# Kernel optimization log

Measured on AMD Instinct MI355X. Metric: run time of the kernel, lower is better.

The kernel has to match this reference:

```python
import jax, jax.numpy as jnp
import numpy as np
from jax import lax

B, S, D_MODEL, H, P = 16, 2048, 512, 8, 128
DEPTH = D_MODEL // H          # 64
C = (S + P - 1) // P          # chunk_size = 16


def _build_table():
    # table[R-1, c, :] = indices of positions assigned to cluster c when R real tokens,
    # padded with R (the padded zero-row index when R == S, else first pad position).
    table = np.zeros((S, P, C), dtype=np.int32)
    cols = np.arange(C)
    for R in range(1, S + 1):
        assign = np.minimum(np.arange(R) * P // R, P - 1)  # nondecreasing
        starts = np.searchsorted(assign, np.arange(P), side='left')
        ends = np.searchsorted(assign, np.arange(P), side='right')
        cand = starts[:, None] + cols[None, :]
        table[R - 1] = np.where(cand < ends[:, None], cand, R)
    return table


def setup_inputs() -> dict:
    key = jax.random.key(0)
    ks = jax.random.split(key, 12)
    def glorot(k, shp):
        fan = shp[-2] + shp[-1]
        return jax.random.normal(k, shp, jnp.float32) * np.sqrt(2.0 / fan).astype(np.float32)
    x = jax.random.normal(ks[0], (B, S, D_MODEL), jnp.float32)
    lengths = jax.random.randint(ks[1], (B,), S // 2, S + 1)
    mask = jnp.arange(S)[None, :] < lengths[:, None]
    return dict(
        x=x, mask=mask,
        wq=glorot(ks[2], (D_MODEL, D_MODEL)),
        wk=glorot(ks[3], (D_MODEL, D_MODEL)),
        wv=glorot(ks[4], (D_MODEL, D_MODEL)),
        e_w=glorot(ks[5], (H, P, C)),
        f_w=glorot(ks[6], (H, P, C)),
        ck1=glorot(ks[7], (1, P, 1, 1)), cb1=jnp.zeros((1,), jnp.float32),
        ck3=glorot(ks[8], (3, P, 1, 1)), cb3=jnp.zeros((1,), jnp.float32),
        ck5=glorot(ks[9], (5, P, 1, 1)), cb5=jnp.zeros((1,), jnp.float32),
        dw=glorot(ks[10], (D_MODEL, D_MODEL)),
        db=jnp.zeros((D_MODEL,), jnp.float32),
        table=jnp.asarray(_build_table()),
    )


def _conv_same(z, kern, bias):
    # z: (N, S, P, 1), kern: (h, P, 1, 1); Keras Conv2D padding='same', stride 1
    return lax.conv_general_dilated(
        z, kern, window_strides=(1, 1), padding='SAME',
        dimension_numbers=('NHWC', 'HWIO', 'NHWC')) + bias


def _forward(x, mask, wq, wk, wv, e_w, f_w, ck1, cb1, ck3, cb3, ck5, cb5, dw, db, table):
    b = x.shape[0]
    split = lambda t: t.reshape(b, S, H, DEPTH).transpose(0, 2, 1, 3)  # (B,H,S,depth)
    q = split(x @ wq)
    k = split(x @ wk)
    v = split(x @ wv)
    pad = ((0, 0), (0, 0), (0, 1), (0, 0))
    k = jnp.pad(k, pad)  # (B,H,S+1,depth) zero pad row at index S
    v = jnp.pad(v, pad)
    real_counts = jnp.clip(jnp.sum(mask.astype(jnp.int32), axis=1), 1, S)
    pos = table[real_counts - 1]                  # (B,P,C) per-batch cluster index table
    gather = jax.vmap(lambda t, idx: t[:, idx])   # gather over seq axis per batch
    k_ch = gather(k, pos)                          # (B,H,P,C,depth)
    v_ch = gather(v, pos)
    k_proj = jnp.einsum('bhpcd,hpc->bhpd', k_ch, e_w)
    v_proj = jnp.einsum('bhpcd,hpc->bhpd', v_ch, f_w)
    scores = jnp.einsum('bhsd,bhpd->bhsp', q, k_proj) / jnp.sqrt(jnp.float32(DEPTH))
    z = scores.reshape(b * H, S, P, 1)
    # mean of the three conv branches (filter heights 1,3,5)
    conv_avg = (_conv_same(z, ck1, cb1) + _conv_same(z, ck3, cb3) + _conv_same(z, ck5, cb5)) / 3.0
    scores = conv_avg.reshape(b, H, S, P)
    w = jax.nn.softmax(scores, axis=-1)
    attn = jnp.einsum('bhsp,bhpd->bhsd', w, v_proj)
    concat = attn.transpose(0, 2, 1, 3).reshape(b, S, D_MODEL)
    return concat @ dw + db


def reference(x, mask, wq, wk, wv, e_w, f_w, ck1, cb1, ck3, cb3, ck5, cb5, dw, db, table):
    return _forward(x, mask, wq, wk, wv, e_w, f_w, ck1, cb1, ck3, cb3, ck5, cb5, dw, db, table)
```

## Files before the change

kernel.cpp:

```cpp
#include <hip/hip_runtime.h>
#include <hip/hip_bf16.h>

#define BN 16
#define SN 2048
#define DM 512
#define HN 8
#define PN 128
#define DEPTH 64
#define CSZ 16

typedef unsigned short u16;
typedef __bf16 bf16x8 __attribute__((ext_vector_type(8)));
typedef float f32x4 __attribute__((ext_vector_type(4)));

#define OFF_QB   0ull
#define OFF_KB   8388608ull
#define OFF_VB   16777216ull
#define OFF_XB   25165824ull
#define OFF_CB   33554432ull
#define OFF_WQT  41943040ull
#define OFF_WKT  42074112ull
#define OFF_WVT  42205184ull
#define OFF_DWT  42336256ull
#define OFF_KP   42467328ull
#define OFF_VPT  43515904ull
#define OFF_KEP  44040192ull
#define OFF_EFF  46661632ull
#define OFF_CNT  46662272ull

__device__ __forceinline__ u16 f2bf(float f) {
    unsigned u = __float_as_uint(f);
    u = (u + 0x7fffu + ((u >> 16) & 1u)) >> 16;
    return (u16)u;
}
__device__ __forceinline__ float b2f(u16 h) {
    return __uint_as_float(((unsigned)h) << 16);
}

__global__ void count_kernel(const void* mask, int* counts) {
    __shared__ int red[256];
    int b = blockIdx.x, tid = threadIdx.x;
    const unsigned char* mb = (const unsigned char*)mask;
    bool is_byte = (mb[1] != 0);
    int local = 0;
    if (is_byte) {
        const unsigned char* row = mb + (size_t)b * SN;
        for (int s = tid; s < SN; s += 256) local += (row[s] != 0);
    } else {
        const int* row = (const int*)mask + (size_t)b * SN;
        for (int s = tid; s < SN; s += 256) local += (row[s] != 0);
    }
    red[tid] = local;
    __syncthreads();
    for (int st = 128; st > 0; st >>= 1) {
        if (tid < st) red[tid] += red[tid + st];
        __syncthreads();
    }
    if (tid == 0) {
        int c = red[0];
        if (c < 1) c = 1;
        if (c > SN) c = SN;
        counts[b] = c;
    }
}

__global__ void eff_kernel(const float* ck1, const float* ck3, const float* ck5, float* eff) {
    int i = threadIdx.x;
    if (i < 640) {
        int t = i >> 7, j = i & 127;
        float v = ck5[t * 128 + j];
        if (t >= 1 && t <= 3) v += ck3[(t - 1) * 128 + j];
        if (t == 2) v += ck1[j];
        eff[i] = v * (1.0f / 3.0f);
    }
}

__global__ void convert_x_kernel(const float* __restrict__ x, u16* __restrict__ xb) {
    size_t i = ((size_t)blockIdx.x * 256 + threadIdx.x) * 4;
    float4 v = *(const float4*)&x[i];
    ushort4 o;
    o.x = f2bf(v.x); o.y = f2bf(v.y); o.z = f2bf(v.z); o.w = f2bf(v.w);
    *(ushort4*)&xb[i] = o;
}

__global__ void convert_wT_kernel(const float* w0, const float* w1, const float* w2, const float* w3,
                                  u16* o0, u16* o1, u16* o2, u16* o3) {
    int z = blockIdx.z;
    const float* W = (z == 0) ? w0 : (z == 1) ? w1 : (z == 2) ? w2 : w3;
    u16* O = (z == 0) ? o0 : (z == 1) ? o1 : (z == 2) ? o2 : o3;
    __shared__ float t[32][33];
    int k0 = blockIdx.y * 32, n0 = blockIdx.x * 32;
    int lx = threadIdx.x & 31, ly = threadIdx.x >> 5;
#pragma unroll
    for (int i = 0; i < 4; i++) t[ly + i * 8][lx] = W[(size_t)(k0 + ly + i * 8) * 512 + n0 + lx];
    __syncthreads();
#pragma unroll
    for (int i = 0; i < 4; i++) O[(size_t)(n0 + ly + i * 8) * 512 + k0 + lx] = f2bf(t[lx][ly + i * 8]);
}

template <int MODE>
__global__ __launch_bounds__(256) void gemm_bf16(const u16* __restrict__ A,
                                                 const u16* W0, const u16* W1, const u16* W2,
                                                 void* O0v, void* O1v, void* O2v,
                                                 const float* __restrict__ bias) {
    __shared__ __align__(16) char smem[32768];
    char* AsB = smem;
    char* BsB = smem + 16384;

    const u16* Wp;
    void* Ov;
    if (MODE == 0) {
        int z = blockIdx.z;
        Wp = (z == 0) ? W0 : (z == 1) ? W1 : W2;
        Ov = (z == 0) ? O0v : (z == 1) ? O1v : O2v;
    } else {
        Wp = W0; Ov = O0v;
    }

    const int m0 = blockIdx.y * 128;
    const int n0 = blockIdx.x * 128;
    const int tid = threadIdx.x;
    const int w = tid >> 6, l = tid & 63;
    const int wm = w >> 1, wn = w & 1;
    const int lr = l >> 3, sp = l & 7;
    const int slog = sp ^ lr;
    const int cl = l & 15, kg = l >> 4;

    const char* Ab = (const char*)A;
    const char* Bb = (const char*)Wp;

    f32x4 acc[4][4];
    const f32x4 z4 = {0.f, 0.f, 0.f, 0.f};
#pragma unroll
    for (int mf = 0; mf < 4; mf++)
#pragma unroll
        for (int nf = 0; nf < 4; nf++) acc[mf][nf] = z4;

    for (int kt = 0; kt < 8; kt++) {
        __syncthreads();
#pragma unroll
        for (int i = 0; i < 4; i++) {
            int c = w * 4 + i;
            const char* ga = Ab + (size_t)(m0 + c * 8 + lr) * 1024 + kt * 128 + slog * 16;
            __builtin_amdgcn_global_load_lds((const __attribute__((address_space(1))) void*)ga,
                                             (__attribute__((address_space(3))) void*)(AsB + c * 1024),
                                             16, 0, 0);
            const char* gb = Bb + (size_t)(n0 + c * 8 + lr) * 1024 + kt * 128 + slog * 16;
            __builtin_amdgcn_global_load_lds((const __attribute__((address_space(1))) void*)gb,
                                             (__attribute__((address_space(3))) void*)(BsB + c * 1024),
                                             16, 0, 0);
        }
        __syncthreads();
#pragma unroll
        for (int ks = 0; ks < 2; ks++) {
            bf16x8 a[4], b[4];
#pragma unroll
            for (int mf = 0; mf < 4; mf++) {
                int row = wm * 64 + mf * 16 + cl;
                a[mf] = *(const bf16x8*)(AsB + row * 128 + (((ks * 4 + kg) ^ (row & 7)) * 16));
            }
#pragma unroll
            for (int nf = 0; nf < 4; nf++) {
                int row = wn * 64 + nf * 16 + cl;
                b[nf] = *(const bf16x8*)(BsB + row * 128 + (((ks * 4 + kg) ^ (row & 7)) * 16));
            }
#pragma unroll
            for (int mf = 0; mf < 4; mf++)
#pragma unroll
                for (int nf = 0; nf < 4; nf++)
                    acc[mf][nf] = __builtin_amdgcn_mfma_f32_16x16x32_bf16(a[mf], b[nf], acc[mf][nf], 0, 0, 0);
        }
    }

    const int rl = l >> 4;
    if (MODE == 0) {
        u16* Ob = (u16*)Ov;
#pragma unroll
        for (int mf = 0; mf < 4; mf++)
#pragma unroll
            for (int nf = 0; nf < 4; nf++) {
                f32x4 v = acc[mf][nf];
                int n = n0 + wn * 64 + nf * 16 + cl;
                int h = n >> 6, d = n & 63;
#pragma unroll
                for (int r = 0; r < 4; r++) {
                    int m = m0 + wm * 64 + mf * 16 + rl * 4 + r;
                    int b = m >> 11, s = m & 2047;
                    Ob[(size_t)((b * HN + h) * SN + s) * DEPTH + d] = f2bf(v[r]);
                }
            }
    } else {
        float* Ob = (float*)Ov;
#pragma unroll
        for (int mf = 0; mf < 4; mf++)
#pragma unroll
            for (int nf = 0; nf < 4; nf++) {
                f32x4 v = acc[mf][nf];
                int n = n0 + wn * 64 + nf * 16 + cl;
                float bs = bias[n];
#pragma unroll
                for (int r = 0; r < 4; r++) {
                    int m = m0 + wm * 64 + mf * 16 + rl * 4 + r;
                    Ob[(size_t)m * 512 + n] = v[r] + bs;
                }
            }
    }
}

__global__ void kvproj_kernel(const u16* __restrict__ Kin, const u16* __restrict__ Vin,
                              const int* __restrict__ table, const int* __restrict__ counts,
                              const float* __restrict__ e_w, const float* __restrict__ f_w,
                              float* __restrict__ kproj, u16* __restrict__ vpT) {
    int p = blockIdx.x;
    int b = blockIdx.y;
    int tid = threadIdx.x;
    int h = tid >> 6, d = tid & 63;
    __shared__ int poss[16];
    __shared__ float ew_s[8][16], fw_s[8][16];
    if (tid < 16) {
        int R = counts[b];
        poss[tid] = table[(size_t)(R - 1) * PN * CSZ + p * CSZ + tid];
    } else if (tid >= 64 && tid < 192) {
        int t2 = tid - 64;
        ew_s[t2 >> 4][t2 & 15] = e_w[(size_t)((t2 >> 4) * PN + p) * CSZ + (t2 & 15)];
    } else if (tid >= 192 && tid < 320) {
        int t2 = tid - 192;
        fw_s[t2 >> 4][t2 & 15] = f_w[(size_t)((t2 >> 4) * PN + p) * CSZ + (t2 & 15)];
    }
    __syncthreads();
    float ka = 0.f, va = 0.f;
    size_t base = (size_t)(b * HN + h) * SN * DEPTH + d;
#pragma unroll
    for (int c = 0; c < CSZ; c++) {
        int idx = poss[c];
        if (idx < SN) {
            float kv = b2f(Kin[base + (size_t)idx * DEPTH]);
            float vv = b2f(Vin[base + (size_t)idx * DEPTH]);
            ka = fmaf(ew_s[h][c], kv, ka);
            va = fmaf(fw_s[h][c], vv, va);
        }
    }
    int bh = b * HN + h;
    kproj[((size_t)bh * PN + p) * DEPTH + d] = ka;
    vpT[(size_t)bh * 8192 + d * 128 + p] = f2bf(va);
}

__global__ __launch_bounds__(256) void ke_kernel(const float* __restrict__ kproj,
                                                 const float* __restrict__ eff,
                                                 u16* __restrict__ keP) {
    int blk = blockIdx.x;
    int bh = blk >> 1;
    int dh = (blk & 1) * 32;
    int tid = threadIdx.x;
    int p = tid & 127;
    int sub = (tid >> 7) * 16;

    __shared__ float kpad[256 * 48];
    __shared__ float ef[640];

    for (int i = tid; i < 256 * 48; i += 256) kpad[i] = 0.f;
    for (int i = tid; i < 640; i += 256) ef[i] = eff[i];
    __syncthreads();
    for (int i = tid; i < 128 * 8; i += 256) {
        int row = i >> 3, c4 = (i & 7) * 4;
        float4 v = *(const float4*)&kproj[(size_t)bh * 8192 + row * 64 + dh + c4];
        *(float4*)&kpad[(64 + row) * 48 + c4] = v;
    }
    __syncthreads();

    float4 acc[5][4];
#pragma unroll
    for (int t = 0; t < 5; t++)
#pragma unroll
        for (int i = 0; i < 4; i++) acc[t][i] = make_float4(0.f, 0.f, 0.f, 0.f);

    for (int j = 0; j < 128; j++) {
        int rr = p + j + 1;
        float4 kv[4];
#pragma unroll
        for (int i = 0; i < 4; i++) kv[i] = *(const float4*)&kpad[rr * 48 + sub + i * 4];
        float w[5];
#pragma unroll
        for (int t = 0; t < 5; t++) w[t] = ef[t * 128 + j];
#pragma unroll
        for (int t = 0; t < 5; t++)
#pragma unroll
            for (int i = 0; i < 4; i++) {
                acc[t][i].x = fmaf(w[t], kv[i].x, acc[t][i].x);
                acc[t][i].y = fmaf(w[t], kv[i].y, acc[t][i].y);
                acc[t][i].z = fmaf(w[t], kv[i].z, acc[t][i].z);
                acc[t][i].w = fmaf(w[t], kv[i].w, acc[t][i].w);
            }
    }

    size_t obase = (size_t)bh * 40960 + (size_t)p * 320;
#pragma unroll
    for (int t = 0; t < 5; t++)
#pragma unroll
        for (int i = 0; i < 4; i++) {
            int d0 = dh + sub + i * 4;
            ushort4 o;
            o.x = f2bf(acc[t][i].x * 0.125f);
            o.y = f2bf(acc[t][i].y * 0.125f);
            o.z = f2bf(acc[t][i].z * 0.125f);
            o.w = f2bf(acc[t][i].w * 0.125f);
            *(ushort4*)&keP[obase + t * 64 + d0] = o;
        }
}

__global__ __launch_bounds__(256) void attn_kernel(const u16* __restrict__ qg,
                                                   const u16* __restrict__ keP,
                                                   const u16* __restrict__ vpT,
                                                   u16* __restrict__ concat) {
    __shared__ __align__(16) char smem[32768];
    char* qswz = smem;
    char* keB = smem + 8704;
    char* wlds = smem;
    char* vps = smem + 16384;

    const int st = blockIdx.x, bh = blockIdx.y;
    const int b = bh >> 3, h = bh & 7;
    const int s0 = st * 64;
    const int tid = threadIdx.x;
    const int w = tid >> 6, l = tid & 63;
    const int cl = l & 15, kg = l >> 4;

    const u16* qb = qg + (size_t)bh * SN * DEPTH;
    for (int i = tid; i < 68 * 8; i += 256) {
        int row = i >> 3, slot = i & 7;
        int srow = s0 + row - 2;
        int4 val = make_int4(0, 0, 0, 0);
        if (srow >= 0 && srow < SN)
            val = *(const int4*)(qb + (size_t)srow * 64 + slot * 8);
        *(int4*)(qswz + row * 128 + ((slot ^ (row & 7)) * 16)) = val;
    }

    f32x4 acc[8];
    const f32x4 z4 = {0.f, 0.f, 0.f, 0.f};
#pragma unroll
    for (int nf = 0; nf < 8; nf++) acc[nf] = z4;

    const char* kePb = (const char*)(keP + (size_t)bh * 40960);
    for (int kt = 0; kt < 5; kt++) {
        __syncthreads();
#pragma unroll
        for (int it = 0; it < 4; it++) {
            int i = it * 256 + tid;
            int p = i >> 3, slot = i & 7;
            const char* src = kePb + 2 * ((size_t)p * 320 + kt * 64) + ((slot ^ (p & 7)) * 16);
            __builtin_amdgcn_global_load_lds((const __attribute__((address_space(1))) void*)src,
                                             (__attribute__((address_space(3))) void*)(keB + i * 16),
                                             16, 0, 0);
        }
        __syncthreads();
#pragma unroll
        for (int ks = 0; ks < 2; ks++) {
            int slot = ks * 4 + kg;
            int arow = w * 16 + kt + cl;
            bf16x8 af = *(const bf16x8*)(qswz + arow * 128 + ((slot ^ (arow & 7)) * 16));
#pragma unroll
            for (int nf = 0; nf < 8; nf++) {
                int prow = nf * 16 + cl;
                bf16x8 bf = *(const bf16x8*)(keB + prow * 128 + ((slot ^ (prow & 7)) * 16));
                acc[nf] = __builtin_amdgcn_mfma_f32_16x16x32_bf16(af, bf, acc[nf], 0, 0, 0);
            }
        }
    }
    __syncthreads();

    const char* vpb = (const char*)(vpT + (size_t)bh * 8192);
#pragma unroll
    for (int it = 0; it < 4; it++) {
        int i = it * 256 + tid;
        int d = i >> 4, slot = i & 15;
        const char* src = vpb + 2 * ((size_t)d * 128) + ((slot ^ (d & 7)) * 16);
        __builtin_amdgcn_global_load_lds((const __attribute__((address_space(1))) void*)src,
                                         (__attribute__((address_space(3))) void*)(vps + i * 16),
                                         16, 0, 0);
    }

    float inv[4];
#pragma unroll
    for (int r = 0; r < 4; r++) {
        float m = acc[0][r];
#pragma unroll
        for (int nf = 1; nf < 8; nf++) m = fmaxf(m, acc[nf][r]);
        m = fmaxf(m, __shfl_xor(m, 1));
        m = fmaxf(m, __shfl_xor(m, 2));
        m = fmaxf(m, __shfl_xor(m, 4));
        m = fmaxf(m, __shfl_xor(m, 8));
        float s = 0.f;
#pragma unroll
        for (int nf = 0; nf < 8; nf++) {
            float e = __expf(acc[nf][r] - m);
            acc[nf][r] = e;
            s += e;
        }
        s += __shfl_xor(s, 1);
        s += __shfl_xor(s, 2);
        s += __shfl_xor(s, 4);
        s += __shfl_xor(s, 8);
        inv[r] = 1.0f / s;
    }
#pragma unroll
    for (int r = 0; r < 4; r++) {
        int row = w * 16 + kg * 4 + r;
#pragma unroll
        for (int nf = 0; nf < 8; nf++) {
            int col = nf * 16 + cl;
            int slot = col >> 3, within = col & 7;
            *(u16*)(wlds + row * 256 + ((slot ^ (row & 7)) * 8 + within) * 2) = f2bf(acc[nf][r] * inv[r]);
        }
    }
    __syncthreads();

    f32x4 acc2[4];
#pragma unroll
    for (int nf = 0; nf < 4; nf++) acc2[nf] = z4;
#pragma unroll
    for (int ks = 0; ks < 4; ks++) {
        int slot = ks * 4 + kg;
        int arow = w * 16 + cl;
        bf16x8 af = *(const bf16x8*)(wlds + arow * 256 + ((slot ^ (arow & 7)) * 16));
#pragma unroll
        for (int nf = 0; nf < 4; nf++) {
            int drow = nf * 16 + cl;
            bf16x8 bf = *(const bf16x8*)(vps + drow * 256 + ((slot ^ (drow & 7)) * 16));
            acc2[nf] = __builtin_amdgcn_mfma_f32_16x16x32_bf16(af, bf, acc2[nf], 0, 0, 0);
        }
    }
#pragma unroll
    for (int nf = 0; nf < 4; nf++) {
#pragma unroll
        for (int r = 0; r < 4; r++) {
            int srow = s0 + w * 16 + kg * 4 + r;
            int d = nf * 16 + cl;
            concat[((size_t)b * SN + srow) * DM + h * 64 + d] = f2bf(acc2[nf][r]);
        }
    }
}

extern "C" void kernel_launch(void* const* d_in, const int* in_sizes, int n_in,
                              void* d_out, int out_size, void* d_ws, size_t ws_size,
                              hipStream_t stream) {
    const float* x = (const float*)d_in[0];
    const void* mask = d_in[1];
    const float* wq = (const float*)d_in[2];
    const float* wk = (const float*)d_in[3];
    const float* wv = (const float*)d_in[4];
    const float* e_w = (const float*)d_in[5];
    const float* f_w = (const float*)d_in[6];
    const float* ck1 = (const float*)d_in[7];
    const float* ck3 = (const float*)d_in[9];
    const float* ck5 = (const float*)d_in[11];
    const float* dw = (const float*)d_in[13];
    const float* db = (const float*)d_in[14];
    const int* table = (const int*)d_in[15];

    float* ws = (float*)d_ws;
    u16* qb = (u16*)(ws + OFF_QB);
    u16* kb = (u16*)(ws + OFF_KB);
    u16* vb = (u16*)(ws + OFF_VB);
    u16* xb = (u16*)(ws + OFF_XB);
    u16* cb = (u16*)(ws + OFF_CB);
    u16* wqT = (u16*)(ws + OFF_WQT);
    u16* wkT = (u16*)(ws + OFF_WKT);
    u16* wvT = (u16*)(ws + OFF_WVT);
    u16* dwT = (u16*)(ws + OFF_DWT);
    float* kp = ws + OFF_KP;
    u16* vpT = (u16*)(ws + OFF_VPT);
    u16* keP = (u16*)(ws + OFF_KEP);
    float* eff = ws + OFF_EFF;
    int* counts = (int*)(ws + OFF_CNT);
    float* out = (float*)d_out;

    count_kernel<<<dim3(16), dim3(256), 0, stream>>>(mask, counts);
    eff_kernel<<<dim3(1), dim3(640), 0, stream>>>(ck1, ck3, ck5, eff);
    convert_x_kernel<<<dim3(16384), dim3(256), 0, stream>>>(x, xb);
    convert_wT_kernel<<<dim3(16, 16, 4), dim3(256), 0, stream>>>(wq, wk, wv, dw, wqT, wkT, wvT, dwT);
    gemm_bf16<0><<<dim3(4, 256, 3), dim3(256), 0, stream>>>(xb, wqT, wkT, wvT, qb, kb, vb, nullptr);
    kvproj_kernel<<<dim3(128, 16), dim3(512), 0, stream>>>(kb, vb, table, counts, e_w, f_w, kp, vpT);
    ke_kernel<<<dim3(256), dim3(256), 0, stream>>>(kp, eff, keP);
    attn_kernel<<<dim3(32, 128), dim3(256), 0, stream>>>(qb, keP, vpT, cb);
    gemm_bf16<1><<<dim3(4, 256, 1), dim3(256), 0, stream>>>(cb, dwT, nullptr, nullptr, out, nullptr, nullptr, db);
}
```

Baseline: 253.5 us.

## Fuse x conversion into merged QKV GEMM and add XCD-aware block swizzling

Removes the separate fp32→bf16 conversion of x by converting inside the QKV GEMM's A-tile load. It also merges the three Q/K/V projections into one kernel that shares each A tile across all three weight matrices, using 512 threads and 64KB of LDS. Block indices for the QKV GEMM, the output GEMM and attention are remapped so neighbouring tiles land on the same XCD for better L2 reuse. The trade-offs are a synchronous fp32 global load on the GEMM critical path and higher register and LDS pressure.

```diff
diff --git a/kernel.cpp b/kernel.cpp
--- a/kernel.cpp
+++ b/kernel.cpp
@@ -16,17 +16,16 @@
 #define OFF_QB   0ull
 #define OFF_KB   8388608ull
 #define OFF_VB   16777216ull
-#define OFF_XB   25165824ull
-#define OFF_CB   33554432ull
-#define OFF_WQT  41943040ull
-#define OFF_WKT  42074112ull
-#define OFF_WVT  42205184ull
-#define OFF_DWT  42336256ull
-#define OFF_KP   42467328ull
-#define OFF_VPT  43515904ull
-#define OFF_KEP  44040192ull
-#define OFF_EFF  46661632ull
-#define OFF_CNT  46662272ull
+#define OFF_CB   25165824ull
+#define OFF_WQT  33554432ull
+#define OFF_WKT  33685504ull
+#define OFF_WVT  33816576ull
+#define OFF_DWT  33947648ull
+#define OFF_KP   34078720ull
+#define OFF_VPT  35127296ull
+#define OFF_KEP  35651584ull
+#define OFF_EFF  38273024ull
+#define OFF_CNT  38273664ull
 
 __device__ __forceinline__ u16 f2bf(float f) {
     unsigned u = __float_as_uint(f);
@@ -35,6 +34,13 @@
 }
 __device__ __forceinline__ float b2f(u16 h) {
     return __uint_as_float(((unsigned)h) << 16);
+}
+
+__device__ __forceinline__ void xcd_decode(int bid, int nmem, int& g, int& j) {
+    int xcd = bid & 7;
+    int t = bid >> 3;
+    j = t % nmem;
+    g = (t / nmem) * 8 + xcd;
 }
 
 __global__ void count_kernel(const void* mask, int* counts) {
@@ -75,14 +81,6 @@
     }
 }
 
-__global__ void convert_x_kernel(const float* __restrict__ x, u16* __restrict__ xb) {
-    size_t i = ((size_t)blockIdx.x * 256 + threadIdx.x) * 4;
-    float4 v = *(const float4*)&x[i];
-    ushort4 o;
-    o.x = f2bf(v.x); o.y = f2bf(v.y); o.z = f2bf(v.z); o.w = f2bf(v.w);
-    *(ushort4*)&xb[i] = o;
-}
-
 __global__ void convert_wT_kernel(const float* w0, const float* w1, const float* w2, const float* w3,
                                   u16* o0, u16* o1, u16* o2, u16* o3) {
     int z = blockIdx.z;
@@ -98,27 +96,119 @@
     for (int i = 0; i < 4; i++) O[(size_t)(n0 + ly + i * 8) * 512 + k0 + lx] = f2bf(t[lx][ly + i * 8]);
 }
 
-template <int MODE>
-__global__ __launch_bounds__(256) void gemm_bf16(const u16* __restrict__ A,
-                                                 const u16* W0, const u16* W1, const u16* W2,
-                                                 void* O0v, void* O1v, void* O2v,
-                                                 const float* __restrict__ bias) {
+__global__ __launch_bounds__(512, 4) void gemm_qkv(const float* __restrict__ X,
+                                                   const u16* __restrict__ WT,
+                                                   u16* __restrict__ Q,
+                                                   u16* __restrict__ K,
+                                                   u16* __restrict__ V) {
+    __shared__ __align__(16) char smem[65536];
+    char* AsB = smem;
+
+    int g, j;
+    xcd_decode(blockIdx.x, 4, g, j);
+    const int m0 = g * 128, n0 = j * 128;
+    const int tid = threadIdx.x;
+    const int w = tid >> 6, l = tid & 63;
+    const int wm = w >> 2, wn = w & 3;
+    const int cl = l & 15, kg = l >> 4;
+
+    f32x4 acc[3][4][2];
+    const f32x4 z4 = {0.f, 0.f, 0.f, 0.f};
+#pragma unroll
+    for (int z = 0; z < 3; z++)
+#pragma unroll
+        for (int mf = 0; mf < 4; mf++)
+#pragma unroll
+            for (int nf = 0; nf < 2; nf++) acc[z][mf][nf] = z4;
+
+    for (int kt = 0; kt < 8; kt++) {
+        __syncthreads();
+#pragma unroll
+        for (int it = 0; it < 2; it++) {
+            int i = it * 512 + tid;
+            int row = i >> 3, slot = i & 7;
+            const float* src = X + (size_t)(m0 + row) * 512 + kt * 64 + ((slot ^ (row & 7)) * 8);
+            float4 v0 = *(const float4*)src;
+            float4 v1 = *(const float4*)(src + 4);
+            int4 pk;
+            pk.x = (int)(f2bf(v0.x) | ((unsigned)f2bf(v0.y) << 16));
+            pk.y = (int)(f2bf(v0.z) | ((unsigned)f2bf(v0.w) << 16));
+            pk.z = (int)(f2bf(v1.x) | ((unsigned)f2bf(v1.y) << 16));
+            pk.w = (int)(f2bf(v1.z) | ((unsigned)f2bf(v1.w) << 16));
+            *(int4*)(AsB + row * 128 + slot * 16) = pk;
+        }
+#pragma unroll
+        for (int z = 0; z < 3; z++) {
+#pragma unroll
+            for (int it = 0; it < 2; it++) {
+                int i = it * 512 + tid;
+                int row = i >> 3, slot = i & 7;
+                const char* src = (const char*)(WT + (size_t)z * 262144 +
+                                                (size_t)(n0 + row) * 512 + kt * 64 + ((slot ^ (row & 7)) * 8));
+                __builtin_amdgcn_global_load_lds((const __attribute__((address_space(1))) void*)src,
+                                                 (__attribute__((address_space(3))) void*)(smem + 16384 + z * 16384 + i * 16),
+                                                 16, 0, 0);
+            }
+        }
+        __syncthreads();
+#pragma unroll
+        for (int ks = 0; ks < 2; ks++) {
+            int slot = ks * 4 + kg;
+            bf16x8 a[4];
+#pragma unroll
+            for (int mf = 0; mf < 4; mf++) {
+                int row = wm * 64 + mf * 16 + cl;
+                a[mf] = *(const bf16x8*)(AsB + row * 128 + ((slot ^ (row & 7)) * 16));
+            }
+#pragma unroll
+            for (int z = 0; z < 3; z++) {
+                const char* Bz = smem + 16384 + z * 16384;
+                bf16x8 b[2];
+#pragma unroll
+                for (int nf = 0; nf < 2; nf++) {
+                    int row = wn * 32 + nf * 16 + cl;
+                    b[nf] = *(const bf16x8*)(Bz + row * 128 + ((slot ^ (row & 7)) * 16));
+                }
+#pragma unroll
+                for (int mf = 0; mf < 4; mf++)
+#pragma unroll
+                    for (int nf = 0; nf < 2; nf++)
+                        acc[z][mf][nf] = __builtin_amdgcn_mfma_f32_16x16x32_bf16(a[mf], b[nf], acc[z][mf][nf], 0, 0, 0);
+            }
+        }
+    }
+
+    const int rl = l >> 4;
+    u16* Ob[3] = {Q, K, V};
+#pragma unroll
+    for (int z = 0; z < 3; z++)
+#pragma unroll
+        for (int mf = 0; mf < 4; mf++)
+#pragma unroll
+            for (int nf = 0; nf < 2; nf++) {
+                f32x4 v = acc[z][mf][nf];
+                int n = n0 + wn * 32 + nf * 16 + cl;
+                int h = n >> 6, d = n & 63;
+#pragma unroll
+                for (int r = 0; r < 4; r++) {
+                    int m = m0 + wm * 64 + mf * 16 + rl * 4 + r;
+                    int b = m >> 11, s = m & 2047;
+                    Ob[z][(size_t)((b * HN + h) * SN + s) * DEPTH + d] = f2bf(v[r]);
+                }
+            }
+}
+
+__global__ __launch_bounds__(256) void gemm_out(const u16* __restrict__ A,
+                                                const u16* __restrict__ WT,
+                                                float* __restrict__ O,
+                                                const float* __restrict__ bias) {
     __shared__ __align__(16) char smem[32768];
     char* AsB = smem;
     char* BsB = smem + 16384;
 
-    const u16* Wp;
-    void* Ov;
-    if (MODE == 0) {
-        int z = blockIdx.z;
-        Wp = (z == 0) ? W0 : (z == 1) ? W1 : W2;
-        Ov = (z == 0) ? O0v : (z == 1) ? O1v : O2v;
-    } else {
-        Wp = W0; Ov = O0v;
-    }
-
-    const int m0 = blockIdx.y * 128;
-    const int n0 = blockIdx.x * 128;
+    int g, j;
+    xcd_decode(blockIdx.x, 4, g, j);
+    const int m0 = g * 128, n0 = j * 128;
     const int tid = threadIdx.x;
     const int w = tid >> 6, l = tid & 63;
     const int wm = w >> 1, wn = w & 1;
@@ -127,7 +217,7 @@
     const int cl = l & 15, kg = l >> 4;
 
     const char* Ab = (const char*)A;
-    const char* Bb = (const char*)Wp;
+    const char* Bb = (const char*)WT;
 
     f32x4 acc[4][4];
     const f32x4 z4 = {0.f, 0.f, 0.f, 0.f};
@@ -173,38 +263,19 @@
     }
 
     const int rl = l >> 4;
-    if (MODE == 0) {
-        u16* Ob = (u16*)Ov;
-#pragma unroll
-        for (int mf = 0; mf < 4; mf++)
-#pragma unroll
-            for (int nf = 0; nf < 4; nf++) {
-                f32x4 v = acc[mf][nf];
-                int n = n0 + wn * 64 + nf * 16 + cl;
-                int h = n >> 6, d = n & 63;
-#pragma unroll
-                for (int r = 0; r < 4; r++) {
-                    int m = m0 + wm * 64 + mf * 16 + rl * 4 + r;
-                    int b = m >> 11, s = m & 2047;
-                    Ob[(size_t)((b * HN + h) * SN + s) * DEPTH + d] = f2bf(v[r]);
-                }
-            }
-    } else {
-        float* Ob = (float*)Ov;
-#pragma unroll
-        for (int mf = 0; mf < 4; mf++)
-#pragma unroll
-            for (int nf = 0; nf < 4; nf++) {
-                f32x4 v = acc[mf][nf];
-                int n = n0 + wn * 64 + nf * 16 + cl;
-                float bs = bias[n];
-#pragma unroll
-                for (int r = 0; r < 4; r++) {
-                    int m = m0 + wm * 64 + mf * 16 + rl * 4 + r;
-                    Ob[(size_t)m * 512 + n] = v[r] + bs;
-                }
-            }
-    }
+#pragma unroll
+    for (int mf = 0; mf < 4; mf++)
+#pragma unroll
+        for (int nf = 0; nf < 4; nf++) {
+            f32x4 v = acc[mf][nf];
+            int n = n0 + wn * 64 + nf * 16 + cl;
+            float bs = bias[n];
+#pragma unroll
+            for (int r = 0; r < 4; r++) {
+                int m = m0 + wm * 64 + mf * 16 + rl * 4 + r;
+                O[(size_t)m * 512 + n] = v[r] + bs;
+            }
+        }
 }
 
 __global__ void kvproj_kernel(const u16* __restrict__ Kin, const u16* __restrict__ Vin,
@@ -318,7 +389,8 @@
     char* wlds = smem;
     char* vps = smem + 16384;
 
-    const int st = blockIdx.x, bh = blockIdx.y;
+    int bh, st;
+    xcd_decode(blockIdx.x, 32, bh, st);
     const int b = bh >> 3, h = bh & 7;
     const int s0 = st * 64;
     const int tid = threadIdx.x;
@@ -461,7 +533,6 @@
     u16* qb = (u16*)(ws + OFF_QB);
     u16* kb = (u16*)(ws + OFF_KB);
     u16* vb = (u16*)(ws + OFF_VB);
-    u16* xb = (u16*)(ws + OFF_XB);
     u16* cb = (u16*)(ws + OFF_CB);
     u16* wqT = (u16*)(ws + OFF_WQT);
     u16* wkT = (u16*)(ws + OFF_WKT);
@@ -476,11 +547,10 @@
 
     count_kernel<<<dim3(16), dim3(256), 0, stream>>>(mask, counts);
     eff_kernel<<<dim3(1), dim3(640), 0, stream>>>(ck1, ck3, ck5, eff);
-    convert_x_kernel<<<dim3(16384), dim3(256), 0, stream>>>(x, xb);
     convert_wT_kernel<<<dim3(16, 16, 4), dim3(256), 0, stream>>>(wq, wk, wv, dw, wqT, wkT, wvT, dwT);
-    gemm_bf16<0><<<dim3(4, 256, 3), dim3(256), 0, stream>>>(xb, wqT, wkT, wvT, qb, kb, vb, nullptr);
+    gemm_qkv<<<dim3(1024), dim3(512), 0, stream>>>(x, wqT, qb, kb, vb);
     kvproj_kernel<<<dim3(128, 16), dim3(512), 0, stream>>>(kb, vb, table, counts, e_w, f_w, kp, vpT);
     ke_kernel<<<dim3(256), dim3(256), 0, stream>>>(kp, eff, keP);
-    attn_kernel<<<dim3(32, 128), dim3(256), 0, stream>>>(qb, keP, vpT, cb);
-    gemm_bf16<1><<<dim3(4, 256, 1), dim3(256), 0, stream>>>(cb, dwT, nullptr, nullptr, out, nullptr, nullptr, db);
-}
+    attn_kernel<<<dim3(4096), dim3(256), 0, stream>>>(qb, keP, vpT, cb);
+    gemm_out<<<dim3(1024), dim3(256), 0, stream>>>(cb, dwT, out, db);
+}
```

Result: faster. 247.6 us (-2.3%).
